# Kernel optimization log

Measured on AMD Instinct MI355X. Metric: run time of the kernel, lower is better.

Reference implementation:

```python
import jax, jax.numpy as jnp
import numpy as np

DIM = 512
HEADS = 8
DIM_HEAD = 64
HIDDEN = HEADS * DIM_HEAD  # 512
SCALE = DIM_HEAD ** (-0.5)
B, T = 8, 8192


def setup_inputs() -> dict:
    key = jax.random.key(0)
    k1, k2, k3, k4, k5 = jax.random.split(key, 5)
    q = jax.random.normal(k1, (B, DIM, T), dtype=jnp.float32)
    # 1x1 Conv1d weights are just [out_ch, in_ch] matrices
    Wq = jax.random.normal(k2, (HIDDEN, DIM), dtype=jnp.float32) * (DIM ** -0.5)
    Wkv = jax.random.normal(k3, (2 * HIDDEN, DIM), dtype=jnp.float32) * (DIM ** -0.5)
    Wout = jax.random.normal(k4, (DIM, HIDDEN), dtype=jnp.float32) * (HIDDEN ** -0.5)
    b_out = jax.random.normal(k5, (DIM,), dtype=jnp.float32) * 0.01
    return {"q": q, "Wq": Wq, "Wkv": Wkv, "Wout": Wout, "b_out": b_out}


def reference(q, Wq, Wkv, Wout, b_out):
    kv_in = q  # kv=None -> self-attention
    # 1x1 conv projections == channel matmuls
    qp = jnp.einsum('oc,bct->bot', Wq, q)          # [B, HIDDEN, T]
    kvp = jnp.einsum('oc,bct->bot', Wkv, kv_in)    # [B, 2*HIDDEN, T]
    k, v = jnp.split(kvp, 2, axis=1)
    split_heads = lambda t: t.reshape(B, HEADS, DIM_HEAD, T)  # b (h c) t -> b h c t
    qh, kh, vh = split_heads(qp), split_heads(k), split_heads(v)
    qh = jax.nn.softmax(qh, axis=-2) * SCALE       # softmax over channel dim
    kh = jax.nn.softmax(kh, axis=-1)               # softmax over time dim
    context = jnp.einsum('bhdn,bhen->bhde', kh, vh)  # [B,H,d,e] small context
    out = jnp.einsum('bhde,bhdn->bhen', context, qh)  # [B,H,e,T]
    out = out.reshape(B, HIDDEN, T)                # b h c t -> b (h c) t
    return jnp.einsum('oc,bct->bot', Wout, out) + b_out[None, :, None]
```

## Files before the change

kernel.cpp:

```cpp
#include <hip/hip_runtime.h>

#define TDIM 8192
#define NB 8
#define CD 512
#define SCALE 0.125f

typedef unsigned int u32;
typedef unsigned short u16;
typedef __bf16 bf16;
typedef bf16 bf16x8 __attribute__((ext_vector_type(8)));
typedef float f32x4 __attribute__((ext_vector_type(4)));
typedef u16 u16x4 __attribute__((ext_vector_type(4)));
typedef u16 u16x8 __attribute__((ext_vector_type(8)));

__device__ __forceinline__ u16 f2bf(float f) {
  u32 u = __float_as_uint(f);
  return (u16)((u + 0x7FFFu + ((u >> 16) & 1u)) >> 16);
}

__device__ __forceinline__ void gload16(const void* g, void* l) {
  __builtin_amdgcn_global_load_lds((const __attribute__((address_space(1))) u32*)g,
                                   (__attribute__((address_space(3))) u32*)l, 16, 0, 0);
}

__global__ __launch_bounds__(256) void k_tq(const float* __restrict__ q, u16* __restrict__ qT) {
  __shared__ float tile[64][65];
  const int b = blockIdx.z, cb = blockIdx.y * 64, tb = blockIdx.x * 64;
  const int tid = threadIdx.x, r = tid >> 2, qd = tid & 3;
  const float* src = q + ((size_t)(b * CD + cb + r)) * TDIM + tb;
#pragma unroll
  for (int j = 0; j < 4; ++j) {
    const float4 v = *(const float4*)(src + j * 16 + qd * 4);
    tile[r][j * 16 + qd * 4 + 0] = v.x;
    tile[r][j * 16 + qd * 4 + 1] = v.y;
    tile[r][j * 16 + qd * 4 + 2] = v.z;
    tile[r][j * 16 + qd * 4 + 3] = v.w;
  }
  __syncthreads();
  u16x8 o0, o1;
#pragma unroll
  for (int i = 0; i < 8; ++i) o0[i] = f2bf(tile[qd * 16 + i][r]);
#pragma unroll
  for (int i = 0; i < 8; ++i) o1[i] = f2bf(tile[qd * 16 + 8 + i][r]);
  u16* dst = qT + ((size_t)b * TDIM + tb + r) * CD + cb + qd * 16;
  *(u16x8*)dst = o0;
  *(u16x8*)(dst + 8) = o1;
}

__global__ __launch_bounds__(256) void k_cast_w(const float* __restrict__ Wq, const float* __restrict__ Wkv,
                                                u16* __restrict__ Wall) {
  const int idx = (blockIdx.x * 256 + threadIdx.x) * 4;
  float4 v;
  if (idx < 512 * 512) v = *(const float4*)(Wq + idx);
  else                 v = *(const float4*)(Wkv + (idx - 512 * 512));
  u16x4 p;
  p[0] = f2bf(v.x); p[1] = f2bf(v.y); p[2] = f2bf(v.z); p[3] = f2bf(v.w);
  *(u16x4*)(Wall + idx) = p;
}

__device__ __forceinline__ void stageA(const u16* __restrict__ Aw, char* buf, int w, int rr, int ch, int kt) {
#pragma unroll
  for (int i = 0; i < 4; ++i)
    gload16(Aw + (size_t)(i * 8 + rr) * CD + kt * 64 + ((ch ^ rr) << 3), buf + (w * 4 + i) * 1024);
}
__device__ __forceinline__ void stageB(const u16* __restrict__ B, char* buf, int w, int rr, int ch, int kt) {
#pragma unroll
  for (int i = 0; i < 2; ++i) {
    const int row = (w * 2 + i) * 8 + rr;
    gload16(B + (size_t)row * CD + kt * 64 + ((ch ^ rr) << 3), buf + 32768 + (w * 2 + i) * 1024);
  }
}

__device__ __forceinline__ void gemm256(const u16* __restrict__ Aw, const u16* __restrict__ B,
                                        char* lds, f32x4 (&acc)[4][4]) {
  const int tid = threadIdx.x, lane = tid & 63, w = tid >> 6;
  const int wr = w >> 1, wc = w & 1;
  const int rr = lane >> 3, ch = lane & 7;
  const int lo16 = lane & 15, hi4 = lane >> 4;
  stageA(Aw, lds, w, rr, ch, 0);          stageB(B, lds, w, rr, ch, 0);
  stageA(Aw, lds + 49152, w, rr, ch, 1);  stageB(B, lds + 49152, w, rr, ch, 1);
#pragma unroll
  for (int kt = 0; kt < 8; ++kt) {
    if (kt < 7) asm volatile("s_waitcnt vmcnt(6)" ::: "memory");
    else        asm volatile("s_waitcnt vmcnt(0)" ::: "memory");
    __builtin_amdgcn_s_barrier();
    char* bc = lds + (kt % 3) * 49152;
    if (kt < 6) {
      char* bn = lds + ((kt + 2) % 3) * 49152;
      stageA(Aw, bn, w, rr, ch, kt + 2);
      stageB(B, bn, w, rr, ch, kt + 2);
    }
#pragma unroll
    for (int ks = 0; ks < 2; ++ks) {
      bf16x8 av[4], bv[4];
#pragma unroll
      for (int am = 0; am < 4; ++am) {
        const int rowA = wr * 64 + am * 16 + lo16;
        av[am] = *(const bf16x8*)(bc + rowA * 128 + ((ks * 64 + hi4 * 16) ^ ((rowA & 7) << 4)));
      }
#pragma unroll
      for (int an = 0; an < 4; ++an) {
        const int rowB = wc * 64 + an * 16 + lo16;
        bv[an] = *(const bf16x8*)(bc + 32768 + rowB * 128 + ((ks * 64 + hi4 * 16) ^ ((rowB & 7) << 4)));
      }
#pragma unroll
      for (int am = 0; am < 4; ++am)
#pragma unroll
        for (int an = 0; an < 4; ++an)
          acc[am][an] = __builtin_amdgcn_mfma_f32_16x16x32_bf16(av[am], bv[an], acc[am][an], 0, 0, 0);
    }
  }
  __syncthreads();
}

__global__ __launch_bounds__(512, 2) void k_proj(const u16* __restrict__ Wall, const u16* __restrict__ qT,
                                                 u16* __restrict__ qhT, float* __restrict__ ctx,
                                                 float* __restrict__ rowsum) {
  __shared__ __align__(16) char LDS[147456];
  const int lid = blockIdx.x;
  const int wg = (lid & 7) * 384 + (lid >> 3);
  const int b = wg / 384, r = wg % 384;
  const int mt = r % 6, nt = r / 6;
  const int t0 = nt * 128;
  const int tid = threadIdx.x, lane = tid & 63, w = tid >> 6;
  const int wr = w >> 1, wc = w & 1, lo16 = lane & 15, hi4 = lane >> 4;
  const bool isQH = mt < 2;
  const int j = mt - 2;
  const u16* Aw;
  if (isQH) Aw = Wall + (size_t)(mt * 256 + w * 32) * CD;
  else      Aw = Wall + (size_t)((w < 4) ? (512 + j * 128 + w * 32)
                                         : (1024 + j * 128 + (w - 4) * 32)) * CD;
  f32x4 acc[4][4] = {};
  gemm256(Aw, qT + ((size_t)b * TDIM + t0) * CD, LDS, acc);
  char* lds = LDS;
  if (isQH) {
    const int row0 = mt * 256;
#pragma unroll
    for (int am = 0; am < 4; ++am)
#pragma unroll
      for (int an = 0; an < 4; ++an)
#pragma unroll
        for (int r2 = 0; r2 < 4; ++r2) acc[am][an][r2] = __expf(acc[am][an][r2]);
#pragma unroll
    for (int an = 0; an < 4; ++an) {
      float s = 0.f;
#pragma unroll
      for (int am = 0; am < 4; ++am)
#pragma unroll
        for (int r2 = 0; r2 < 4; ++r2) s += acc[am][an][r2];
      s += __shfl_xor(s, 16);
      s += __shfl_xor(s, 32);
      const float inv = SCALE / s;
#pragma unroll
      for (int am = 0; am < 4; ++am)
#pragma unroll
        for (int r2 = 0; r2 < 4; ++r2) acc[am][an][r2] *= inv;
    }
#pragma unroll
    for (int am = 0; am < 4; ++am)
#pragma unroll
      for (int an = 0; an < 4; ++an) {
        const int tl = wc * 64 + an * 16 + lo16;
        const int cb2 = (wr * 64 + am * 16 + hi4 * 4) * 2;
        u16x4 p;
#pragma unroll
        for (int r2 = 0; r2 < 4; ++r2) p[r2] = f2bf(acc[am][an][r2]);
        *(u16x4*)(lds + tl * 512 + ((cb2 & ~15) ^ ((tl & 7) << 4)) + (cb2 & 8)) = p;
      }
    __syncthreads();
#pragma unroll
    for (int pp = 0; pp < 8; ++pp) {
      const int tr = pp * 16 + (tid >> 5), chk = tid & 31;
      const uint4 val = *(const uint4*)(lds + tr * 512 + ((chk * 16) ^ ((tr & 7) << 4)));
      *(uint4*)(qhT + ((size_t)b * TDIM + t0 + tr) * CD + row0 + chk * 8) = val;
    }
  } else {
    if (wr < 2) {
#pragma unroll
      for (int am = 0; am < 4; ++am)
#pragma unroll
        for (int an = 0; an < 4; ++an)
#pragma unroll
          for (int r2 = 0; r2 < 4; ++r2) acc[am][an][r2] = __expf(acc[am][an][r2]);
#pragma unroll
      for (int am = 0; am < 4; ++am)
#pragma unroll
        for (int r2 = 0; r2 < 4; ++r2) {
          float s = acc[am][0][r2] + acc[am][1][r2] + acc[am][2][r2] + acc[am][3][r2];
          s += __shfl_xor(s, 1); s += __shfl_xor(s, 2);
          s += __shfl_xor(s, 4); s += __shfl_xor(s, 8);
          if (lo16 == 0)
            unsafeAtomicAdd(rowsum + b * CD + j * 128 + wr * 64 + am * 16 + hi4 * 4 + r2, s);
        }
    }
#pragma unroll
    for (int am = 0; am < 4; ++am)
#pragma unroll
      for (int an = 0; an < 4; ++an) {
        const int tl2 = (wc * 64 + an * 16 + lo16) * 2;
#pragma unroll
        for (int r2 = 0; r2 < 4; ++r2) {
          const int cl = wr * 64 + am * 16 + hi4 * 4 + r2;
          *(u16*)(lds + cl * 256 + ((tl2 & ~15) ^ ((cl & 7) << 4)) + (tl2 & 15)) = f2bf(acc[am][an][r2]);
        }
      }
    __syncthreads();
    const int hw = w >> 2, d0 = (w & 1) * 32, e0 = ((w >> 1) & 1) * 32;
    f32x4 cacc[2][2] = {};
#pragma unroll
    for (int tk = 0; tk < 4; ++tk) {
      bf16x8 ea[2], vv[2];
#pragma unroll
      for (int dm = 0; dm < 2; ++dm) {
        const int rowE = hw * 64 + d0 + dm * 16 + lo16;
        ea[dm] = *(const bf16x8*)(lds + rowE * 256 + ((tk * 64 + hi4 * 16) ^ ((rowE & 7) << 4)));
      }
#pragma unroll
      for (int de = 0; de < 2; ++de) {
        const int rowV = 128 + hw * 64 + e0 + de * 16 + lo16;
        vv[de] = *(const bf16x8*)(lds + rowV * 256 + ((tk * 64 + hi4 * 16) ^ ((rowV & 7) << 4)));
      }
#pragma unroll
      for (int dm = 0; dm < 2; ++dm)
#pragma unroll
        for (int de = 0; de < 2; ++de)
          cacc[dm][de] = __builtin_amdgcn_mfma_f32_16x16x32_bf16(ea[dm], vv[de], cacc[dm][de], 0, 0, 0);
    }
    float* cdst = ctx + ((size_t)(b * 8 + j * 2 + hw)) * 4096;
#pragma unroll
    for (int dm = 0; dm < 2; ++dm)
#pragma unroll
      for (int de = 0; de < 2; ++de)
#pragma unroll
        for (int r2 = 0; r2 < 4; ++r2)
          unsafeAtomicAdd(cdst + (d0 + dm * 16 + hi4 * 4 + r2) * 64 + e0 + de * 16 + lo16,
                          cacc[dm][de][r2]);
  }
}

__global__ __launch_bounds__(256) void k_weff(const float* __restrict__ Wout, const float* __restrict__ ctx,
                                              const float* __restrict__ rowsum, u16* __restrict__ Weff) {
  __shared__ float cn[64][65];
  __shared__ float rsin[64];
  const int bh = blockIdx.y, b = bh >> 3, h = bh & 7;
  const int o0 = blockIdx.x * 64;
  const int tid = threadIdx.x;
  if (tid < 64) rsin[tid] = 1.f / rowsum[b * CD + h * 64 + tid];
  __syncthreads();
  const float* csrc = ctx + (size_t)bh * 4096;
#pragma unroll
  for (int i = 0; i < 16; ++i) {
    const int idx = tid + 256 * i;
    cn[idx >> 6][idx & 63] = csrc[idx] * rsin[idx >> 6];
  }
  __syncthreads();
  const int o = o0 + (tid >> 2), dq = (tid & 3) * 16;
  const float* wrow = Wout + (size_t)o * CD + h * 64;
  float a[16] = {};
  for (int e2 = 0; e2 < 64; ++e2) {
    const float wv = wrow[e2];
#pragma unroll
    for (int i = 0; i < 16; ++i) a[i] += wv * cn[dq + i][e2];
  }
  u16x8 p0, p1;
#pragma unroll
  for (int i = 0; i < 8; ++i) { p0[i] = f2bf(a[i]); p1[i] = f2bf(a[8 + i]); }
  u16* dst = Weff + ((size_t)(b * CD + o)) * CD + h * 64 + dq;
  *(u16x8*)dst = p0;
  *(u16x8*)(dst + 8) = p1;
}

__global__ __launch_bounds__(512, 2) void k_final(const u16* __restrict__ Weff, const u16* __restrict__ qhT,
                                                  const float* __restrict__ bias, float* __restrict__ out) {
  __shared__ __align__(16) char LDS[147456];
  const int lid = blockIdx.x;
  const int wg = (lid & 7) * 128 + (lid >> 3);
  const int b = wg >> 7, r = wg & 127;
  const int mt = r & 1, nt = r >> 1;
  const int row0 = mt * 256, t0 = nt * 128;
  const int tid = threadIdx.x, lane = tid & 63, w = tid >> 6;
  const int wr = w >> 1, wc = w & 1, lo16 = lane & 15, hi4 = lane >> 4;
  const u16* Aw = Weff + ((size_t)(b * CD + row0 + w * 32)) * CD;
  f32x4 acc[4][4] = {};
  gemm256(Aw, qhT + ((size_t)b * TDIM + t0) * CD, LDS, acc);
#pragma unroll
  for (int am = 0; am < 4; ++am)
#pragma unroll
    for (int r2 = 0; r2 < 4; ++r2) {
      const int o = row0 + wr * 64 + am * 16 + hi4 * 4 + r2;
      const float bo = bias[o];
      float* orow = out + ((size_t)(b * CD + o)) * TDIM + t0 + wc * 64 + lo16;
#pragma unroll
      for (int an = 0; an < 4; ++an)
        orow[an * 16] = acc[am][an][r2] + bo;
    }
}

extern "C" void kernel_launch(void* const* d_in, const int* in_sizes, int n_in,
                              void* d_out, int out_size, void* d_ws, size_t ws_size,
                              hipStream_t stream) {
  const float* q    = (const float*)d_in[0];
  const float* Wq   = (const float*)d_in[1];
  const float* Wkv  = (const float*)d_in[2];
  const float* Wout = (const float*)d_in[3];
  const float* bout = (const float*)d_in[4];
  float* out = (float*)d_out;
  char* ws = (char*)d_ws;
  const size_t SZ = (size_t)NB * CD * TDIM * 2;
  u16* qT  = (u16*)ws;
  u16* qhT = (u16*)(ws + SZ);
  char* base = ws + 2 * SZ;
  u16* Wall   = (u16*)base;
  float* ctx  = (float*)(base + (2u << 20));
  float* rsum = (float*)(base + (3u << 20));
  u16* Weff   = (u16*)(base + (4u << 20));
  (void)in_sizes; (void)n_in; (void)out_size; (void)ws_size;

  hipMemsetAsync(base + (2u << 20), 0, 2u << 20, stream);
  k_tq    <<<dim3(128, 8, 8), 256, 0, stream>>>(q, qT);
  k_cast_w<<<dim3(768), 256, 0, stream>>>(Wq, Wkv, Wall);
  k_proj  <<<dim3(3072), 512, 0, stream>>>(Wall, qT, qhT, ctx, rsum);
  k_weff  <<<dim3(8, 64), 256, 0, stream>>>(Wout, ctx, rsum, Weff);
  k_final <<<dim3(1024), 512, 0, stream>>>(Weff, qhT, bout, out);
}
```

Before: 252.7 us.

## Load GEMM A-operand directly from global memory, shrink LDS to raise occupancy

The shared GEMM routine stops staging the weight (A) tiles through LDS and instead has each wave read its A fragments straight from global memory into registers, leaving only the B tile triple-buffered in LDS. This cuts LDS use per block from 144KB to 64KB/48KB, and launch bounds are raised to allow 4 blocks per CU. The aim is higher occupancy and less LDS traffic. In exchange, the A loads become synchronous, uncoalesced-ish global reads inside the inner loop, with no prefetch and duplication across the two waves sharing a row group. Register pressure under the tighter launch bound may also cause spills.

```diff
diff --git a/kernel.cpp b/kernel.cpp
--- a/kernel.cpp
+++ b/kernel.cpp
@@ -58,50 +58,40 @@
   *(u16x4*)(Wall + idx) = p;
 }
 
-__device__ __forceinline__ void stageA(const u16* __restrict__ Aw, char* buf, int w, int rr, int ch, int kt) {
-#pragma unroll
-  for (int i = 0; i < 4; ++i)
-    gload16(Aw + (size_t)(i * 8 + rr) * CD + kt * 64 + ((ch ^ rr) << 3), buf + (w * 4 + i) * 1024);
-}
 __device__ __forceinline__ void stageB(const u16* __restrict__ B, char* buf, int w, int rr, int ch, int kt) {
 #pragma unroll
   for (int i = 0; i < 2; ++i) {
     const int row = (w * 2 + i) * 8 + rr;
-    gload16(B + (size_t)row * CD + kt * 64 + ((ch ^ rr) << 3), buf + 32768 + (w * 2 + i) * 1024);
-  }
-}
-
-__device__ __forceinline__ void gemm256(const u16* __restrict__ Aw, const u16* __restrict__ B,
-                                        char* lds, f32x4 (&acc)[4][4]) {
+    gload16(B + (size_t)row * CD + kt * 64 + ((ch ^ rr) << 3), buf + (w * 2 + i) * 1024);
+  }
+}
+
+__device__ __forceinline__ void gemm_ag(const u16* __restrict__ Aw ,
+                                        const u16* __restrict__ B, char* lds, f32x4 (&acc)[4][4]) {
   const int tid = threadIdx.x, lane = tid & 63, w = tid >> 6;
-  const int wr = w >> 1, wc = w & 1;
+  const int wc = w & 1;
   const int rr = lane >> 3, ch = lane & 7;
   const int lo16 = lane & 15, hi4 = lane >> 4;
-  stageA(Aw, lds, w, rr, ch, 0);          stageB(B, lds, w, rr, ch, 0);
-  stageA(Aw, lds + 49152, w, rr, ch, 1);  stageB(B, lds + 49152, w, rr, ch, 1);
+  stageB(B, lds, w, rr, ch, 0);
+  stageB(B, lds + 16384, w, rr, ch, 1);
 #pragma unroll
   for (int kt = 0; kt < 8; ++kt) {
-    if (kt < 7) asm volatile("s_waitcnt vmcnt(6)" ::: "memory");
+    if (kt < 7) asm volatile("s_waitcnt vmcnt(2)" ::: "memory");
     else        asm volatile("s_waitcnt vmcnt(0)" ::: "memory");
     __builtin_amdgcn_s_barrier();
-    char* bc = lds + (kt % 3) * 49152;
-    if (kt < 6) {
-      char* bn = lds + ((kt + 2) % 3) * 49152;
-      stageA(Aw, bn, w, rr, ch, kt + 2);
-      stageB(B, bn, w, rr, ch, kt + 2);
-    }
+    char* bc = lds + (kt % 3) * 16384;
+    if (kt < 6)
+      stageB(B, lds + ((kt + 2) % 3) * 16384, w, rr, ch, kt + 2);
 #pragma unroll
     for (int ks = 0; ks < 2; ++ks) {
       bf16x8 av[4], bv[4];
 #pragma unroll
-      for (int am = 0; am < 4; ++am) {
-        const int rowA = wr * 64 + am * 16 + lo16;
-        av[am] = *(const bf16x8*)(bc + rowA * 128 + ((ks * 64 + hi4 * 16) ^ ((rowA & 7) << 4)));
-      }
+      for (int am = 0; am < 4; ++am)
+        av[am] = *(const bf16x8*)(Aw + (size_t)(am * 16 + lo16) * CD + kt * 64 + ks * 32 + hi4 * 8);
 #pragma unroll
       for (int an = 0; an < 4; ++an) {
         const int rowB = wc * 64 + an * 16 + lo16;
-        bv[an] = *(const bf16x8*)(bc + 32768 + rowB * 128 + ((ks * 64 + hi4 * 16) ^ ((rowB & 7) << 4)));
+        bv[an] = *(const bf16x8*)(bc + rowB * 128 + ((ks * 64 + hi4 * 16) ^ ((rowB & 7) << 4)));
       }
 #pragma unroll
       for (int am = 0; am < 4; ++am)
@@ -113,10 +103,10 @@
   __syncthreads();
 }
 
-__global__ __launch_bounds__(512, 2) void k_proj(const u16* __restrict__ Wall, const u16* __restrict__ qT,
+__global__ __launch_bounds__(512, 4) void k_proj(const u16* __restrict__ Wall, const u16* __restrict__ qT,
                                                  u16* __restrict__ qhT, float* __restrict__ ctx,
                                                  float* __restrict__ rowsum) {
-  __shared__ __align__(16) char LDS[147456];
+  __shared__ __align__(16) char LDS[65536];
   const int lid = blockIdx.x;
   const int wg = (lid & 7) * 384 + (lid >> 3);
   const int b = wg / 384, r = wg % 384;
@@ -127,11 +117,11 @@
   const bool isQH = mt < 2;
   const int j = mt - 2;
   const u16* Aw;
-  if (isQH) Aw = Wall + (size_t)(mt * 256 + w * 32) * CD;
-  else      Aw = Wall + (size_t)((w < 4) ? (512 + j * 128 + w * 32)
-                                         : (1024 + j * 128 + (w - 4) * 32)) * CD;
+  if (isQH)        Aw = Wall + (size_t)(mt * 256 + wr * 64) * CD;
+  else if (wr < 2) Aw = Wall + (size_t)(512 + j * 128 + wr * 64) * CD;
+  else             Aw = Wall + (size_t)(1024 + j * 128 + (wr - 2) * 64) * CD;
   f32x4 acc[4][4] = {};
-  gemm256(Aw, qT + ((size_t)b * TDIM + t0) * CD, LDS, acc);
+  gemm_ag(Aw, qT + ((size_t)b * TDIM + t0) * CD, LDS, acc);
   char* lds = LDS;
   if (isQH) {
     const int row0 = mt * 256;
@@ -270,9 +260,9 @@
   *(u16x8*)(dst + 8) = p1;
 }
 
-__global__ __launch_bounds__(512, 2) void k_final(const u16* __restrict__ Weff, const u16* __restrict__ qhT,
+__global__ __launch_bounds__(512, 4) void k_final(const u16* __restrict__ Weff, const u16* __restrict__ qhT,
                                                   const float* __restrict__ bias, float* __restrict__ out) {
-  __shared__ __align__(16) char LDS[147456];
+  __shared__ __align__(16) char LDS[49152];
   const int lid = blockIdx.x;
   const int wg = (lid & 7) * 128 + (lid >> 3);
   const int b = wg >> 7, r = wg & 127;
@@ -280,9 +270,9 @@
   const int row0 = mt * 256, t0 = nt * 128;
   const int tid = threadIdx.x, lane = tid & 63, w = tid >> 6;
   const int wr = w >> 1, wc = w & 1, lo16 = lane & 15, hi4 = lane >> 4;
-  const u16* Aw = Weff + ((size_t)(b * CD + row0 + w * 32)) * CD;
+  const u16* Aw = Weff + ((size_t)(b * CD + row0 + wr * 64)) * CD;
   f32x4 acc[4][4] = {};
-  gemm256(Aw, qhT + ((size_t)b * TDIM + t0) * CD, LDS, acc);
+  gemm_ag(Aw, qhT + ((size_t)b * TDIM + t0) * CD, LDS, acc);
 #pragma unroll
   for (int am = 0; am < 4; ++am)
 #pragma unroll
```

New measurement: 417.5 us. +65.2%, slower.

## Halve GEMM K-tile to 32 and shrink LDS so two blocks fit per CU

Applied to the files above, without the earlier changes.

The shared GEMM routine now stages K in 32-wide slices instead of 64, using 16 iterations with a 3-stage ring. Each stage is 24 KB, so the LDS buffers in k_proj and k_final drop from 144 KB to 72 KB. The goal is to let two 512-thread workgroups share a CU, matching the launch bound of 2, so one block's memory latency can hide behind the other's compute. The XOR swizzle on LDS rows is removed, which can cause LDS bank conflicts on the 64-byte-strided fragment reads, and the shorter K slices mean more barriers per tile.

```diff
diff --git a/kernel.cpp b/kernel.cpp
--- a/kernel.cpp
+++ b/kernel.cpp
@@ -58,57 +58,46 @@
   *(u16x4*)(Wall + idx) = p;
 }
 
-__device__ __forceinline__ void stageA(const u16* __restrict__ Aw, char* buf, int w, int rr, int ch, int kt) {
-#pragma unroll
-  for (int i = 0; i < 4; ++i)
-    gload16(Aw + (size_t)(i * 8 + rr) * CD + kt * 64 + ((ch ^ rr) << 3), buf + (w * 4 + i) * 1024);
-}
-__device__ __forceinline__ void stageB(const u16* __restrict__ B, char* buf, int w, int rr, int ch, int kt) {
-#pragma unroll
-  for (int i = 0; i < 2; ++i) {
-    const int row = (w * 2 + i) * 8 + rr;
-    gload16(B + (size_t)row * CD + kt * 64 + ((ch ^ rr) << 3), buf + 32768 + (w * 2 + i) * 1024);
-  }
-}
-
-__device__ __forceinline__ void gemm256(const u16* __restrict__ Aw, const u16* __restrict__ B,
-                                        char* lds, f32x4 (&acc)[4][4]) {
+__device__ __forceinline__ void stage32(const u16* __restrict__ Aw, const u16* __restrict__ B8,
+                                        char* buf, int w, int lane, int kt) {
+  const int r4 = lane >> 2, c4 = lane & 3;
+  const size_t go = (size_t)r4 * CD + kt * 32 + c4 * 8;
+  gload16(Aw + go, buf + w * 2048);
+  gload16(Aw + 16 * CD + go, buf + w * 2048 + 1024);
+  gload16(B8 + (size_t)(w * 16) * CD + go, buf + 16384 + w * 1024);
+}
+
+__device__ __forceinline__ void gemm256(const u16* __restrict__ Aw ,
+                                        const u16* __restrict__ B8, char* lds, f32x4 (&acc)[4][4]) {
   const int tid = threadIdx.x, lane = tid & 63, w = tid >> 6;
   const int wr = w >> 1, wc = w & 1;
-  const int rr = lane >> 3, ch = lane & 7;
   const int lo16 = lane & 15, hi4 = lane >> 4;
-  stageA(Aw, lds, w, rr, ch, 0);          stageB(B, lds, w, rr, ch, 0);
-  stageA(Aw, lds + 49152, w, rr, ch, 1);  stageB(B, lds + 49152, w, rr, ch, 1);
-#pragma unroll
-  for (int kt = 0; kt < 8; ++kt) {
-    if (kt < 7) asm volatile("s_waitcnt vmcnt(6)" ::: "memory");
-    else        asm volatile("s_waitcnt vmcnt(0)" ::: "memory");
+  stage32(Aw, B8, lds, w, lane, 0);
+  stage32(Aw, B8, lds + 24576, w, lane, 1);
+#pragma unroll
+  for (int kt = 0; kt < 16; ++kt) {
+    if (kt < 15) asm volatile("s_waitcnt vmcnt(3)" ::: "memory");
+    else         asm volatile("s_waitcnt vmcnt(0)" ::: "memory");
     __builtin_amdgcn_s_barrier();
-    char* bc = lds + (kt % 3) * 49152;
-    if (kt < 6) {
-      char* bn = lds + ((kt + 2) % 3) * 49152;
-      stageA(Aw, bn, w, rr, ch, kt + 2);
-      stageB(B, bn, w, rr, ch, kt + 2);
-    }
-#pragma unroll
-    for (int ks = 0; ks < 2; ++ks) {
-      bf16x8 av[4], bv[4];
-#pragma unroll
-      for (int am = 0; am < 4; ++am) {
-        const int rowA = wr * 64 + am * 16 + lo16;
-        av[am] = *(const bf16x8*)(bc + rowA * 128 + ((ks * 64 + hi4 * 16) ^ ((rowA & 7) << 4)));
-      }
-#pragma unroll
-      for (int an = 0; an < 4; ++an) {
-        const int rowB = wc * 64 + an * 16 + lo16;
-        bv[an] = *(const bf16x8*)(bc + 32768 + rowB * 128 + ((ks * 64 + hi4 * 16) ^ ((rowB & 7) << 4)));
-      }
-#pragma unroll
-      for (int am = 0; am < 4; ++am)
-#pragma unroll
-        for (int an = 0; an < 4; ++an)
-          acc[am][an] = __builtin_amdgcn_mfma_f32_16x16x32_bf16(av[am], bv[an], acc[am][an], 0, 0, 0);
-    }
+    char* bc = lds + (kt % 3) * 24576;
+    if (kt < 14)
+      stage32(Aw, B8, lds + ((kt + 2) % 3) * 24576, w, lane, kt + 2);
+    bf16x8 av[4], bv[4];
+#pragma unroll
+    for (int am = 0; am < 4; ++am) {
+      const int rowA = wr * 64 + am * 16 + lo16;
+      av[am] = *(const bf16x8*)(bc + rowA * 64 + hi4 * 16);
+    }
+#pragma unroll
+    for (int an = 0; an < 4; ++an) {
+      const int rowB = wc * 64 + an * 16 + lo16;
+      bv[an] = *(const bf16x8*)(bc + 16384 + rowB * 64 + hi4 * 16);
+    }
+#pragma unroll
+    for (int am = 0; am < 4; ++am)
+#pragma unroll
+      for (int an = 0; an < 4; ++an)
+        acc[am][an] = __builtin_amdgcn_mfma_f32_16x16x32_bf16(av[am], bv[an], acc[am][an], 0, 0, 0);
   }
   __syncthreads();
 }
@@ -116,7 +105,7 @@
 __global__ __launch_bounds__(512, 2) void k_proj(const u16* __restrict__ Wall, const u16* __restrict__ qT,
                                                  u16* __restrict__ qhT, float* __restrict__ ctx,
                                                  float* __restrict__ rowsum) {
-  __shared__ __align__(16) char LDS[147456];
+  __shared__ __align__(16) char LDS[73728];
   const int lid = blockIdx.x;
   const int wg = (lid & 7) * 384 + (lid >> 3);
   const int b = wg / 384, r = wg % 384;
@@ -127,9 +116,9 @@
   const bool isQH = mt < 2;
   const int j = mt - 2;
   const u16* Aw;
-  if (isQH) Aw = Wall + (size_t)(mt * 256 + w * 32) * CD;
-  else      Aw = Wall + (size_t)((w < 4) ? (512 + j * 128 + w * 32)
-                                         : (1024 + j * 128 + (w - 4) * 32)) * CD;
+  if (isQH)       Aw = Wall + (size_t)(mt * 256 + w * 32) * CD;
+  else if (w < 4) Aw = Wall + (size_t)(512 + j * 128 + w * 32) * CD;
+  else            Aw = Wall + (size_t)(1024 + j * 128 + (w - 4) * 32) * CD;
   f32x4 acc[4][4] = {};
   gemm256(Aw, qT + ((size_t)b * TDIM + t0) * CD, LDS, acc);
   char* lds = LDS;
@@ -272,7 +261,7 @@
 
 __global__ __launch_bounds__(512, 2) void k_final(const u16* __restrict__ Weff, const u16* __restrict__ qhT,
                                                   const float* __restrict__ bias, float* __restrict__ out) {
-  __shared__ __align__(16) char LDS[147456];
+  __shared__ __align__(16) char LDS[73728];
   const int lid = blockIdx.x;
   const int wg = (lid & 7) * 128 + (lid >> 3);
   const int b = wg >> 7, r = wg & 127;
```

New measurement: 251.1 us. Within noise of the previous version (-0.7%).
